# Kernel tuning notes

Measured on AMD Instinct MI355X. Metric: run time of the kernel, lower is better.

## Reference

```python
import jax, jax.numpy as jnp
import numpy as np

NCLASSES = 100
ALPHA = 1.0
CLIP = False


def setup_inputs() -> dict:
    key = jax.random.key(0)
    k1, k2, k3 = jax.random.split(key, 3)
    N, D, C = 8192, 10000, NCLASSES
    encoded = jax.random.normal(k1, (N, D), dtype=jnp.float32)
    class_hvs = jax.random.normal(k2, (C, D), dtype=jnp.float32)
    targets = jax.random.randint(k3, (N,), 0, C, dtype=jnp.int64)
    return {"encoded": encoded, "class_hvs": class_hvs, "targets": targets}


def reference(encoded, class_hvs, targets):
    # Cosine-similarity scores: [N, C]
    scores = jnp.matmul(encoded, class_hvs.T)
    norm_enc = jnp.linalg.norm(encoded, axis=1)        # [N]
    norm_cls = jnp.linalg.norm(class_hvs, axis=1)      # [C]
    scores = scores / (norm_enc[:, None] * norm_cls[None, :])

    # Training-path perceptron update (torch code runs this under no_grad)
    preds = jnp.argmax(scores, axis=1)                 # [N]
    wrong = (targets != preds).astype(encoded.dtype)   # [N]
    enc_wrong = encoded * wrong[:, None]               # masked rows, zeros elsewhere

    # sum of misclassified encodings grouped by true label / predicted label
    add_t = jax.ops.segment_sum(enc_wrong, targets, num_segments=NCLASSES) * ALPHA
    sub_p = jax.ops.segment_sum(enc_wrong, preds, num_segments=NCLASSES)
    if CLIP:
        add_t = jnp.clip(add_t, -1.0, 1.0)
        sub_p = jnp.clip(sub_p, -1.0, 1.0)
    new_class_hvs = class_hvs + add_t * ALPHA - sub_p * ALPHA
    new_class_hvs = jax.lax.stop_gradient(new_class_hvs)

    return scores, new_class_hvs
```

## Files before the change

### kernel.cpp

```cpp
#include <hip/hip_runtime.h>
#include <hip/hip_bf16.h>
#include <math.h>

#define NROWS 8192
#define DDIM  10000
#define NCLS  100
#define LISTCAP 512

#define KSPLIT 8
#define KS32   314
#define BM 128

#define SCORES_N (NROWS*NCLS)
#define NCHUNK8 1256
#define BP_CHUNKS (NCHUNK8*128)

#define WS_NORMCLS 0
#define WS_NRM     128
#define WS_SCP     (WS_NRM + KSPLIT*NROWS)
#define WS_CNT_T   (WS_SCP + KSPLIT*SCORES_N)
#define WS_CNT_P   (WS_CNT_T + 128)
#define WS_LIST_T  (WS_CNT_P + 128)
#define WS_LIST_P  (WS_LIST_T + NCLS*LISTCAP)
#define WS_BPH     (WS_LIST_P + NCLS*LISTCAP)
#define WS_BPL     (WS_BPH + BP_CHUNKS*4)

typedef _Float16 f16;
typedef f16 f16x8 __attribute__((ext_vector_type(8)));
typedef float f32x4 __attribute__((ext_vector_type(4)));

#define SBAR()  __builtin_amdgcn_s_barrier()
#define SCHED() __builtin_amdgcn_sched_barrier(0)

__global__ __launch_bounds__(256) void cls_norms(const float* __restrict__ cls,
                                                 float* __restrict__ ws)
{
    if (blockIdx.x == 0) ((int*)ws)[WS_CNT_T + threadIdx.x] = 0;

    int c = blockIdx.x;
    const float* row = cls + (size_t)c * DDIM;
    float s = 0.f;
    for (int d = threadIdx.x; d < DDIM; d += 256) {
        float v = row[d];
        s = fmaf(v, v, s);
    }
    #pragma unroll
    for (int off = 32; off; off >>= 1) s += __shfl_xor(s, off, 64);
    __shared__ float red[4];
    int w = threadIdx.x >> 6, l = threadIdx.x & 63;
    if (l == 0) red[w] = s;
    __syncthreads();
    if (threadIdx.x == 0) {
        float t = red[0] + red[1] + red[2] + red[3];
        ws[WS_NORMCLS + c] = sqrtf(t);
    }
}

__global__ __launch_bounds__(256) void prep_b(const float* __restrict__ cls,
                                              float* __restrict__ ws)
{
    int c = blockIdx.x * 256 + threadIdx.x;
    if (c >= BP_CHUNKS) return;
    int col = c & 127, k8 = c >> 7;
    f16x8 hi, lo;
    #pragma unroll
    for (int j = 0; j < 8; ++j) {
        int k = k8 * 8 + j;
        float v = (col < NCLS && k < DDIM) ? cls[(size_t)col * DDIM + k] : 0.f;
        f16 h = (f16)v;
        hi[j] = h;
        lo[j] = (f16)(v - (float)h);
    }
    ((f16x8*)(ws + WS_BPH))[c] = hi;
    ((f16x8*)(ws + WS_BPL))[c] = lo;
}

__global__ __launch_bounds__(256, 2) void gemm_mfma(const float* __restrict__ enc,
                                                    float* __restrict__ ws)
{
    __shared__ f16 Bh[2][4*128*8], Bl[2][4*128*8];

    int tid = threadIdx.x;
    int w = __builtin_amdgcn_readfirstlane(tid >> 6);
    int l = tid & 63;
    int lane15 = l & 15, lg = l >> 4;
    int r0 = blockIdx.x * BM;
    int ky = blockIdx.y;
    int s_beg = (KS32 * ky) / KSPLIT;
    int s_end = (KS32 * (ky + 1)) / KSPLIT;

    const float* aptr0 = enc + (size_t)(r0 + w * 32 + lane15) * DDIM;
    const float* aptr1 = aptr0 + (size_t)16 * DDIM;
    const f16* bph = (const f16*)(ws + WS_BPH);
    const f16* bpl = (const f16*)(ws + WS_BPL);

    f32x4 acc[2][7] = {};
    float nsq0 = 0.f, nsq1 = 0.f;

    float4 a00, a01, a10, a11;
    f16x8 bsh0, bsh1, bsl0, bsl1;

    #define LOAD_A(S) do {                                               \
        int k_ = (S) * 32 + lg * 8;                                      \
        int ka_ = (k_ + 4 <= DDIM) ? k_ : 0;                             \
        int kb_ = (k_ + 8 <= DDIM) ? (k_ + 4) : 0;                       \
        a00 = *(const float4*)(aptr0 + ka_);                             \
        a01 = *(const float4*)(aptr0 + kb_);                             \
        a10 = *(const float4*)(aptr1 + ka_);                             \
        a11 = *(const float4*)(aptr1 + kb_);                             \
    } while (0)

    #define LOAD_B(S) do {                                               \
        size_t base_ = ((size_t)((S) * 4 + w) * 128) * 8;                \
        bsh0 = *(const f16x8*)(bph + base_ + (size_t)l * 8);             \
        bsh1 = *(const f16x8*)(bph + base_ + (size_t)(l + 64) * 8);      \
        bsl0 = *(const f16x8*)(bpl + base_ + (size_t)l * 8);             \
        bsl1 = *(const f16x8*)(bpl + base_ + (size_t)(l + 64) * 8);      \
    } while (0)

    LOAD_A(s_beg);
    LOAD_B(s_beg);

    for (int S = s_beg; S < s_end; ++S) {
        int cur = S & 1;

        int kb = S * 32 + lg * 8;
        bool tail = (kb + 8 > DDIM);
        f16x8 ah0, al0, ah1, al1;
        {
            float v[8] = {a00.x, a00.y, a00.z, a00.w, a01.x, a01.y, a01.z, a01.w};
            if (tail) {
                #pragma unroll
                for (int j = 0; j < 8; ++j) if (kb + j >= DDIM) v[j] = 0.f;
            }
            #pragma unroll
            for (int j = 0; j < 8; ++j) {
                f16 h = (f16)v[j];
                ah0[j] = h;
                al0[j] = (f16)(v[j] - (float)h);
                nsq0 = fmaf(v[j], v[j], nsq0);
            }
        }
        {
            float v[8] = {a10.x, a10.y, a10.z, a10.w, a11.x, a11.y, a11.z, a11.w};
            if (tail) {
                #pragma unroll
                for (int j = 0; j < 8; ++j) if (kb + j >= DDIM) v[j] = 0.f;
            }
            #pragma unroll
            for (int j = 0; j < 8; ++j) {
                f16 h = (f16)v[j];
                ah1[j] = h;
                al1[j] = (f16)(v[j] - (float)h);
                nsq1 = fmaf(v[j], v[j], nsq1);
            }
        }

        {
            int sl0 = w * 128 + (l ^ w);
            *(f16x8*)&Bh[cur][sl0 * 8] = bsh0;
            *(f16x8*)&Bh[cur][(sl0 + 64) * 8] = bsh1;
            *(f16x8*)&Bl[cur][sl0 * 8] = bsl0;
            *(f16x8*)&Bl[cur][(sl0 + 64) * 8] = bsl1;
        }

        {
            int Sn = (S + 1 < s_end) ? (S + 1) : S;
            LOAD_A(Sn);
            LOAD_B(Sn);
        }

        SCHED();
        asm volatile("s_waitcnt lgkmcnt(0)" ::: "memory");
        SBAR();
        SCHED();

        #pragma unroll
        for (int nt = 0; nt < 7; ++nt) {
            int colS = (nt * 16 + lane15) ^ lg;
            f16x8 bh = *(const f16x8*)&Bh[cur][(lg * 128 + colS) * 8];
            f16x8 bl = *(const f16x8*)&Bl[cur][(lg * 128 + colS) * 8];
            acc[0][nt] = __builtin_amdgcn_mfma_f32_16x16x32_f16(ah0, bh, acc[0][nt], 0, 0, 0);
            acc[0][nt] = __builtin_amdgcn_mfma_f32_16x16x32_f16(al0, bh, acc[0][nt], 0, 0, 0);
            acc[0][nt] = __builtin_amdgcn_mfma_f32_16x16x32_f16(ah0, bl, acc[0][nt], 0, 0, 0);
            acc[1][nt] = __builtin_amdgcn_mfma_f32_16x16x32_f16(ah1, bh, acc[1][nt], 0, 0, 0);
            acc[1][nt] = __builtin_amdgcn_mfma_f32_16x16x32_f16(al1, bh, acc[1][nt], 0, 0, 0);
            acc[1][nt] = __builtin_amdgcn_mfma_f32_16x16x32_f16(ah1, bl, acc[1][nt], 0, 0, 0);
        }
    }

    float* scp = ws + WS_SCP + (size_t)ky * SCORES_N;
    #pragma unroll
    for (int mt = 0; mt < 2; ++mt) {
        #pragma unroll
        for (int nt = 0; nt < 7; ++nt) {
            int gcol = nt * 16 + lane15;
            if (gcol < NCLS) {
                #pragma unroll
                for (int j = 0; j < 4; ++j) {
                    int grow = r0 + w * 32 + mt * 16 + lg * 4 + j;
                    scp[(size_t)grow * NCLS + gcol] = acc[mt][nt][j];
                }
            }
        }
    }

    nsq0 += __shfl_xor(nsq0, 16, 64);
    nsq0 += __shfl_xor(nsq0, 32, 64);
    nsq1 += __shfl_xor(nsq1, 16, 64);
    nsq1 += __shfl_xor(nsq1, 32, 64);
    if (l < 16) {
        ws[WS_NRM + (size_t)ky * NROWS + r0 + w * 32 + l] = nsq0;
        ws[WS_NRM + (size_t)ky * NROWS + r0 + w * 32 + 16 + l] = nsq1;
    }
}

__global__ __launch_bounds__(256) void finalize(const int* __restrict__ targets,
                                                float* __restrict__ out,
                                                float* __restrict__ ws)
{
    int w = threadIdx.x >> 6, l = threadIdx.x & 63;
    int row = blockIdx.x * 4 + w;
    const float* scp = ws + WS_SCP;

    float n2 = 0.f;
    #pragma unroll
    for (int ky = 0; ky < KSPLIT; ++ky) n2 += ws[WS_NRM + (size_t)ky * NROWS + row];
    float ne = sqrtf(n2);

    float best; int bi;
    {
        int c = l;
        float dsum = 0.f;
        #pragma unroll
        for (int ky = 0; ky < KSPLIT; ++ky)
            dsum += scp[(size_t)ky * SCORES_N + (size_t)row * NCLS + c];
        float s = dsum / (ne * ws[WS_NORMCLS + c]);
        out[(size_t)row * NCLS + c] = s;
        best = s; bi = c;
    }
    if (l + 64 < NCLS) {
        int c = l + 64;
        float dsum = 0.f;
        #pragma unroll
        for (int ky = 0; ky < KSPLIT; ++ky)
            dsum += scp[(size_t)ky * SCORES_N + (size_t)row * NCLS + c];
        float s = dsum / (ne * ws[WS_NORMCLS + c]);
        out[(size_t)row * NCLS + c] = s;
        if (s > best) { best = s; bi = c; }
    }
    #pragma unroll
    for (int off = 32; off; off >>= 1) {
        float ov = __shfl_xor(best, off, 64);
        int   oi = __shfl_xor(bi, off, 64);
        if (ov > best || (ov == best && oi < bi)) { best = ov; bi = oi; }
    }
    if (l == 0) {
        int tgt = targets[row];
        if (tgt != bi) {
            int* wsi = (int*)ws;
            int p1 = atomicAdd(wsi + WS_CNT_T + tgt, 1);
            if (p1 < LISTCAP) wsi[WS_LIST_T + tgt * LISTCAP + p1] = row;
            int p2 = atomicAdd(wsi + WS_CNT_P + bi, 1);
            if (p2 < LISTCAP) wsi[WS_LIST_P + bi * LISTCAP + p2] = row;
        }
    }
}

__global__ __launch_bounds__(256) void update(const float* __restrict__ enc,
                                              const float* __restrict__ cls,
                                              float* __restrict__ out,
                                              const float* __restrict__ ws)
{
    __shared__ int lstT[LISTCAP], lstP[LISTCAP];
    int c = blockIdx.x;
    const int* wsi = (const int*)ws;
    int nt = wsi[WS_CNT_T + c]; nt = nt < LISTCAP ? nt : LISTCAP;
    int np = wsi[WS_CNT_P + c]; np = np < LISTCAP ? np : LISTCAP;
    for (int i = threadIdx.x; i < nt; i += 256) lstT[i] = wsi[WS_LIST_T + c * LISTCAP + i];
    for (int i = threadIdx.x; i < np; i += 256) lstP[i] = wsi[WS_LIST_P + c * LISTCAP + i];
    __syncthreads();

    int d4 = blockIdx.y * 256 + threadIdx.x;
    if (d4 >= DDIM / 4) return;
    const float4* enc4 = (const float4*)enc;
    const float4* cls4 = (const float4*)cls;

    float4 ac0 = make_float4(0.f, 0.f, 0.f, 0.f);
    float4 ac1 = make_float4(0.f, 0.f, 0.f, 0.f);
    int i = 0;
    #pragma unroll 2
    for (; i + 2 <= nt; i += 2) {
        float4 e0 = enc4[(size_t)lstT[i] * (DDIM / 4) + d4];
        float4 e1 = enc4[(size_t)lstT[i + 1] * (DDIM / 4) + d4];
        ac0.x += e0.x; ac0.y += e0.y; ac0.z += e0.z; ac0.w += e0.w;
        ac1.x += e1.x; ac1.y += e1.y; ac1.z += e1.z; ac1.w += e1.w;
    }
    if (i < nt) {
        float4 e0 = enc4[(size_t)lstT[i] * (DDIM / 4) + d4];
        ac0.x += e0.x; ac0.y += e0.y; ac0.z += e0.z; ac0.w += e0.w;
    }
    i = 0;
    #pragma unroll 2
    for (; i + 2 <= np; i += 2) {
        float4 e0 = enc4[(size_t)lstP[i] * (DDIM / 4) + d4];
        float4 e1 = enc4[(size_t)lstP[i + 1] * (DDIM / 4) + d4];
        ac0.x -= e0.x; ac0.y -= e0.y; ac0.z -= e0.z; ac0.w -= e0.w;
        ac1.x -= e1.x; ac1.y -= e1.y; ac1.z -= e1.z; ac1.w -= e1.w;
    }
    if (i < np) {
        float4 e0 = enc4[(size_t)lstP[i] * (DDIM / 4) + d4];
        ac0.x -= e0.x; ac0.y -= e0.y; ac0.z -= e0.z; ac0.w -= e0.w;
    }

    float4 cv = cls4[(size_t)c * (DDIM / 4) + d4];
    float4 r = make_float4(cv.x + ac0.x + ac1.x, cv.y + ac0.y + ac1.y,
                           cv.z + ac0.z + ac1.z, cv.w + ac0.w + ac1.w);
    ((float4*)out)[SCORES_N / 4 + (size_t)c * (DDIM / 4) + d4] = r;
}

extern "C" void kernel_launch(void* const* d_in, const int* in_sizes, int n_in,
                              void* d_out, int out_size, void* d_ws, size_t ws_size,
                              hipStream_t stream)
{
    const float* enc = (const float*)d_in[0];
    const float* cls = (const float*)d_in[1];
    const int*   tgt = (const int*)d_in[2];
    float* out = (float*)d_out;
    float* ws  = (float*)d_ws;

    cls_norms<<<NCLS, 256, 0, stream>>>(cls, ws);
    prep_b<<<(BP_CHUNKS + 255) / 256, 256, 0, stream>>>(cls, ws);

    dim3 g1(NROWS / BM, KSPLIT);
    gemm_mfma<<<g1, 256, 0, stream>>>(enc, ws);

    finalize<<<NROWS / 4, 256, 0, stream>>>(tgt, out, ws);

    dim3 g3(NCLS, (DDIM / 4 + 255) / 256);
    update<<<g3, 256, 0, stream>>>(enc, cls, out, ws);
}
```

Before: 242.6 us.

## Double GEMM K-step to 64 per iteration and sort misclassified row lists

The split-K MFMA GEMM now processes 64 K elements per loop iteration instead of 32, doubling the LDS B tile and the A register prefetch. This halves the number of barriers and loop overheads per block and gives more MFMA work between syncs, at the cost of higher register and LDS pressure. A new bitonic sort kernel orders each per-class misclassified row list, which makes the update kernel's summation order deterministic and its row accesses ordered, but adds an extra kernel launch.

```diff
diff --git a/kernel.cpp b/kernel.cpp
--- a/kernel.cpp
+++ b/kernel.cpp
@@ -8,7 +8,7 @@
 #define LISTCAP 512
 
 #define KSPLIT 8
-#define KS32   314
+#define KS64   157
 #define BM 128
 
 #define SCORES_N (NROWS*NCLS)
@@ -78,7 +78,7 @@
 __global__ __launch_bounds__(256, 2) void gemm_mfma(const float* __restrict__ enc,
                                                     float* __restrict__ ws)
 {
-    __shared__ f16 Bh[2][4*128*8], Bl[2][4*128*8];
+    __shared__ f16 Bh[2][8*128*8], Bl[2][8*128*8];
 
     int tid = threadIdx.x;
     int w = __builtin_amdgcn_readfirstlane(tid >> 6);
@@ -86,8 +86,8 @@
     int lane15 = l & 15, lg = l >> 4;
     int r0 = blockIdx.x * BM;
     int ky = blockIdx.y;
-    int s_beg = (KS32 * ky) / KSPLIT;
-    int s_end = (KS32 * (ky + 1)) / KSPLIT;
+    int s_beg = (KS64 * ky) / KSPLIT;
+    int s_end = (KS64 * (ky + 1)) / KSPLIT;
 
     const float* aptr0 = enc + (size_t)(r0 + w * 32 + lane15) * DDIM;
     const float* aptr1 = aptr0 + (size_t)16 * DDIM;
@@ -97,25 +97,35 @@
     f32x4 acc[2][7] = {};
     float nsq0 = 0.f, nsq1 = 0.f;
 
-    float4 a00, a01, a10, a11;
-    f16x8 bsh0, bsh1, bsl0, bsl1;
+    float4 ar[8];
+    f16x8 bsh[2][2], bsl[2][2];
 
     #define LOAD_A(S) do {                                               \
-        int k_ = (S) * 32 + lg * 8;                                      \
-        int ka_ = (k_ + 4 <= DDIM) ? k_ : 0;                             \
-        int kb_ = (k_ + 8 <= DDIM) ? (k_ + 4) : 0;                       \
-        a00 = *(const float4*)(aptr0 + ka_);                             \
-        a01 = *(const float4*)(aptr0 + kb_);                             \
-        a10 = *(const float4*)(aptr1 + ka_);                             \
-        a11 = *(const float4*)(aptr1 + kb_);                             \
+        int kA_ = (S) * 64 + lg * 8;                                     \
+        int kB_ = kA_ + 32;                                              \
+        int a0_ = (kA_ + 4 <= DDIM) ? kA_ : 0;                           \
+        int a1_ = (kA_ + 8 <= DDIM) ? (kA_ + 4) : 0;                     \
+        int b0_ = (kB_ + 4 <= DDIM) ? kB_ : 0;                           \
+        int b1_ = (kB_ + 8 <= DDIM) ? (kB_ + 4) : 0;                     \
+        ar[0] = *(const float4*)(aptr0 + a0_);                           \
+        ar[1] = *(const float4*)(aptr0 + a1_);                           \
+        ar[2] = *(const float4*)(aptr0 + b0_);                           \
+        ar[3] = *(const float4*)(aptr0 + b1_);                           \
+        ar[4] = *(const float4*)(aptr1 + a0_);                           \
+        ar[5] = *(const float4*)(aptr1 + a1_);                           \
+        ar[6] = *(const float4*)(aptr1 + b0_);                           \
+        ar[7] = *(const float4*)(aptr1 + b1_);                           \
     } while (0)
 
     #define LOAD_B(S) do {                                               \
-        size_t base_ = ((size_t)((S) * 4 + w) * 128) * 8;                \
-        bsh0 = *(const f16x8*)(bph + base_ + (size_t)l * 8);             \
-        bsh1 = *(const f16x8*)(bph + base_ + (size_t)(l + 64) * 8);      \
-        bsl0 = *(const f16x8*)(bpl + base_ + (size_t)l * 8);             \
-        bsl1 = *(const f16x8*)(bpl + base_ + (size_t)(l + 64) * 8);      \
+        _Pragma("unroll")                                                \
+        for (int j_ = 0; j_ < 2; ++j_) {                                 \
+            size_t base_ = ((size_t)((S) * 8 + 2 * w + j_) * 128) * 8;   \
+            bsh[j_][0] = *(const f16x8*)(bph + base_ + (size_t)l * 8);   \
+            bsh[j_][1] = *(const f16x8*)(bph + base_ + (size_t)(l + 64) * 8); \
+            bsl[j_][0] = *(const f16x8*)(bpl + base_ + (size_t)l * 8);   \
+            bsl[j_][1] = *(const f16x8*)(bpl + base_ + (size_t)(l + 64) * 8); \
+        }                                                                \
     } while (0)
 
     LOAD_A(s_beg);
@@ -124,44 +134,38 @@
     for (int S = s_beg; S < s_end; ++S) {
         int cur = S & 1;
 
-        int kb = S * 32 + lg * 8;
-        bool tail = (kb + 8 > DDIM);
-        f16x8 ah0, al0, ah1, al1;
-        {
-            float v[8] = {a00.x, a00.y, a00.z, a00.w, a01.x, a01.y, a01.z, a01.w};
-            if (tail) {
+        f16x8 ah[2][2], al[2][2];
+        #pragma unroll
+        for (int r = 0; r < 2; ++r) {
+            float& nsq = r ? nsq1 : nsq0;
+            #pragma unroll
+            for (int ks = 0; ks < 2; ++ks) {
+                float4 p0 = ar[r * 4 + ks * 2], p1 = ar[r * 4 + ks * 2 + 1];
+                float v[8] = {p0.x, p0.y, p0.z, p0.w, p1.x, p1.y, p1.z, p1.w};
+                int kb = S * 64 + ks * 32 + lg * 8;
+                if (kb + 8 > DDIM) {
+                    #pragma unroll
+                    for (int j = 0; j < 8; ++j) if (kb + j >= DDIM) v[j] = 0.f;
+                }
                 #pragma unroll
-                for (int j = 0; j < 8; ++j) if (kb + j >= DDIM) v[j] = 0.f;
+                for (int j = 0; j < 8; ++j) {
+                    f16 h = (f16)v[j];
+                    ah[r][ks][j] = h;
+                    al[r][ks][j] = (f16)(v[j] - (float)h);
+                    nsq = fmaf(v[j], v[j], nsq);
+                }
             }
-            #pragma unroll
-            for (int j = 0; j < 8; ++j) {
-                f16 h = (f16)v[j];
-                ah0[j] = h;
-                al0[j] = (f16)(v[j] - (float)h);
-                nsq0 = fmaf(v[j], v[j], nsq0);
-            }
-        }
-        {
-            float v[8] = {a10.x, a10.y, a10.z, a10.w, a11.x, a11.y, a11.z, a11.w};
-            if (tail) {
-                #pragma unroll
-                for (int j = 0; j < 8; ++j) if (kb + j >= DDIM) v[j] = 0.f;
-            }
-            #pragma unroll
-            for (int j = 0; j < 8; ++j) {
-                f16 h = (f16)v[j];
-                ah1[j] = h;
-                al1[j] = (f16)(v[j] - (float)h);
-                nsq1 = fmaf(v[j], v[j], nsq1);
-            }
-        }
-
-        {
-            int sl0 = w * 128 + (l ^ w);
-            *(f16x8*)&Bh[cur][sl0 * 8] = bsh0;
-            *(f16x8*)&Bh[cur][(sl0 + 64) * 8] = bsh1;
-            *(f16x8*)&Bl[cur][sl0 * 8] = bsl0;
-            *(f16x8*)&Bl[cur][(sl0 + 64) * 8] = bsl1;
+        }
+
+        #pragma unroll
+        for (int j = 0; j < 2; ++j) {
+            int kg = 2 * w + j;
+            int s0 = kg * 128 + (l ^ kg);
+            int s1 = kg * 128 + ((l + 64) ^ kg);
+            *(f16x8*)&Bh[cur][s0 * 8] = bsh[j][0];
+            *(f16x8*)&Bh[cur][s1 * 8] = bsh[j][1];
+            *(f16x8*)&Bl[cur][s0 * 8] = bsl[j][0];
+            *(f16x8*)&Bl[cur][s1 * 8] = bsl[j][1];
         }
 
         {
@@ -176,16 +180,20 @@
         SCHED();
 
         #pragma unroll
-        for (int nt = 0; nt < 7; ++nt) {
-            int colS = (nt * 16 + lane15) ^ lg;
-            f16x8 bh = *(const f16x8*)&Bh[cur][(lg * 128 + colS) * 8];
-            f16x8 bl = *(const f16x8*)&Bl[cur][(lg * 128 + colS) * 8];
-            acc[0][nt] = __builtin_amdgcn_mfma_f32_16x16x32_f16(ah0, bh, acc[0][nt], 0, 0, 0);
-            acc[0][nt] = __builtin_amdgcn_mfma_f32_16x16x32_f16(al0, bh, acc[0][nt], 0, 0, 0);
-            acc[0][nt] = __builtin_amdgcn_mfma_f32_16x16x32_f16(ah0, bl, acc[0][nt], 0, 0, 0);
-            acc[1][nt] = __builtin_amdgcn_mfma_f32_16x16x32_f16(ah1, bh, acc[1][nt], 0, 0, 0);
-            acc[1][nt] = __builtin_amdgcn_mfma_f32_16x16x32_f16(al1, bh, acc[1][nt], 0, 0, 0);
-            acc[1][nt] = __builtin_amdgcn_mfma_f32_16x16x32_f16(ah1, bl, acc[1][nt], 0, 0, 0);
+        for (int ks = 0; ks < 2; ++ks) {
+            int kg = ks * 4 + lg;
+            #pragma unroll
+            for (int nt = 0; nt < 7; ++nt) {
+                int colS = (nt * 16 + lane15) ^ kg;
+                f16x8 bh = *(const f16x8*)&Bh[cur][(kg * 128 + colS) * 8];
+                f16x8 bl = *(const f16x8*)&Bl[cur][(kg * 128 + colS) * 8];
+                acc[0][nt] = __builtin_amdgcn_mfma_f32_16x16x32_f16(ah[0][ks], bh, acc[0][nt], 0, 0, 0);
+                acc[0][nt] = __builtin_amdgcn_mfma_f32_16x16x32_f16(al[0][ks], bh, acc[0][nt], 0, 0, 0);
+                acc[0][nt] = __builtin_amdgcn_mfma_f32_16x16x32_f16(ah[0][ks], bl, acc[0][nt], 0, 0, 0);
+                acc[1][nt] = __builtin_amdgcn_mfma_f32_16x16x32_f16(ah[1][ks], bh, acc[1][nt], 0, 0, 0);
+                acc[1][nt] = __builtin_amdgcn_mfma_f32_16x16x32_f16(al[1][ks], bh, acc[1][nt], 0, 0, 0);
+                acc[1][nt] = __builtin_amdgcn_mfma_f32_16x16x32_f16(ah[1][ks], bl, acc[1][nt], 0, 0, 0);
+            }
         }
     }
 
@@ -267,6 +275,39 @@
     }
 }
 
+__global__ __launch_bounds__(256) void sort_lists(float* __restrict__ ws)
+{
+    __shared__ int buf[LISTCAP];
+    int* wsi = (int*)ws;
+    int c = blockIdx.x >> 1;
+    int which = blockIdx.x & 1;
+    int* list = wsi + (which ? WS_LIST_P + c * LISTCAP : WS_LIST_T + c * LISTCAP);
+    int n = wsi[(which ? WS_CNT_P : WS_CNT_T) + c];
+    n = n < LISTCAP ? n : LISTCAP;
+
+    #pragma unroll
+    for (int t = threadIdx.x; t < LISTCAP; t += 256)
+        buf[t] = (t < n) ? list[t] : 0x7FFFFFFF;
+    __syncthreads();
+
+    for (int k = 2; k <= LISTCAP; k <<= 1) {
+        for (int j = k >> 1; j > 0; j >>= 1) {
+            #pragma unroll
+            for (int t = threadIdx.x; t < LISTCAP; t += 256) {
+                int ixj = t ^ j;
+                if (ixj > t) {
+                    int a = buf[t], b = buf[ixj];
+                    bool up = ((t & k) == 0);
+                    if ((a > b) == up) { buf[t] = b; buf[ixj] = a; }
+                }
+            }
+            __syncthreads();
+        }
+    }
+
+    for (int t = threadIdx.x; t < n; t += 256) list[t] = buf[t];
+}
+
 __global__ __launch_bounds__(256) void update(const float* __restrict__ enc,
                                               const float* __restrict__ cls,
                                               float* __restrict__ out,
@@ -337,6 +378,8 @@
 
     finalize<<<NROWS / 4, 256, 0, stream>>>(tgt, out, ws);
 
+    sort_lists<<<NCLS * 2, 256, 0, stream>>>(ws);
+
     dim3 g3(NCLS, (DDIM / 4 + 255) / 256);
     update<<<g3, 256, 0, stream>>>(enc, cls, out, ws);
 }
```

After: 256.9 us. 1.06x slower.
